# Performance work log

Hardware: AMD Instinct MI355X
Metric: run time of the kernel (lower is better)

## Reference

```python
import jax, jax.numpy as jnp
import numpy as np

ALPHA = 0.2  # tf.nn.leaky_relu default

def leaky(x):
    return jnp.where(x >= 0, x, ALPHA * x)

def segment_softmax(score, seg, num_segments):
    m = jax.ops.segment_max(score, seg, num_segments=num_segments)
    e = jnp.exp(score - m[seg])
    denom = jax.ops.segment_sum(e, seg, num_segments=num_segments)
    return e / denom[seg]

def setup_inputs() -> dict:
    key = jax.random.key(0)
    ks = jax.random.split(key, 8)
    E, NE, NR, D, U = 500000, 100000, 1000, 128, 128
    return {
        "h_index": jax.random.randint(ks[0], (E,), 0, NE),
        "r_index": jax.random.randint(ks[1], (E,), 0, NR),
        "t_index": jax.random.randint(ks[2], (E,), 0, NE),
        "entity_embeddings": jax.random.normal(ks[3], (NE, D), jnp.float32),
        "relation_embeddings": jax.random.normal(ks[4], (NR, D), jnp.float32),
        "W": jax.random.normal(ks[5], (3 * D, U), jnp.float32) * 0.05,
        "a": jax.random.normal(ks[6], (U, 1), jnp.float32) * 0.1,
        "a_b": jnp.zeros((1,), jnp.float32),
        "bias": jnp.zeros((U,), jnp.float32),
    }

def reference(h_index, r_index, t_index, entity_embeddings, relation_embeddings, W, a, a_b, bias):
    num_entities = entity_embeddings.shape[0]
    h = entity_embeddings[h_index]          # [E, D]
    r = relation_embeddings[r_index]        # [E, D]
    t = entity_embeddings[t_index]          # [E, D]
    feats = jnp.concatenate([h, r, t], axis=-1) @ W  # [E, U]
    # att_kernel Dense(1, activation=leaky_relu), then wrapped again in att_activation
    score = leaky(leaky(feats @ a + a_b))[:, 0]      # [E]
    alpha = segment_softmax(score, h_index, num_entities)
    msg = feats * alpha[:, None]                     # gcn_mapper: edge features * weight
    reduced = jax.ops.segment_sum(msg, h_index, num_segments=num_entities)  # [NE, U]
    out = reduced + bias                             # identity_updater returns reduced_msg
    return jax.nn.relu(out)
```

## Files before the change

### kernel.cpp

```cpp
#include <hip/hip_runtime.h>
#include <hip/hip_bf16.h>

#define ALPHA2 0.04f

typedef __attribute__((ext_vector_type(8))) short short8;
typedef __attribute__((ext_vector_type(4))) float floatx4;
typedef __attribute__((ext_vector_type(8))) unsigned short ushort8;

__device__ __forceinline__ unsigned short f2bf(float f) {
    unsigned u = __float_as_uint(f);
    unsigned r = (u + 0x7fffu + ((u >> 16) & 1u)) >> 16;
    return (unsigned short)r;
}
__device__ __forceinline__ float bf2f(unsigned short h) {
    return __uint_as_float((unsigned)h << 16);
}

__global__ void k_prep(const float* __restrict__ W, unsigned short* __restrict__ Wt,
                       int* __restrict__ count, int NE) {
    int idx = blockIdx.x * blockDim.x + threadIdx.x;
    if (idx < 384 * 128) {
        int k = idx >> 7, n = idx & 127;
        Wt[n * 384 + k] = f2bf(W[idx]);
    }
    if (idx < NE) count[idx] = 0;
}

#define LDA 136

__device__ __forceinline__ void gemm_phase(
        const unsigned short* Ash, unsigned short* Wsh,
        int rowbase, int nrows, int wave, int lane, int tid,
        const float* __restrict__ avec,
        unsigned short* __restrict__ OutB, float* __restrict__ svec) {
    int m16 = lane & 15, quad = lane >> 4;
    int rs = wave * 32;

    floatx4 acc[2][8];
    #pragma unroll
    for (int i = 0; i < 2; ++i)
        #pragma unroll
        for (int j = 0; j < 8; ++j) acc[i][j] = (floatx4){0.f, 0.f, 0.f, 0.f};

    #pragma unroll
    for (int kc = 0; kc < 4; ++kc) {
        short8 af[2], bf[8];
        #pragma unroll
        for (int i = 0; i < 2; ++i)
            af[i] = *(const short8*)(Ash + (rs + i * 16 + m16) * LDA + kc * 32 + quad * 8);
        #pragma unroll
        for (int j = 0; j < 8; ++j)
            bf[j] = *(const short8*)(Wsh + (j * 16 + m16) * LDA + kc * 32 + quad * 8);
        #pragma unroll
        for (int i = 0; i < 2; ++i)
            #pragma unroll
            for (int j = 0; j < 8; ++j)
                acc[i][j] = __builtin_amdgcn_mfma_f32_16x16x32_bf16(af[i], bf[j], acc[i][j], 0, 0, 0);
    }

    float av[8];
    #pragma unroll
    for (int j = 0; j < 8; ++j) av[j] = avec[j * 16 + m16];
    #pragma unroll
    for (int i = 0; i < 2; ++i) {
        #pragma unroll
        for (int reg = 0; reg < 4; ++reg) {
            int row = rowbase + rs + i * 16 + quad * 4 + reg;
            float part = 0.f;
            #pragma unroll
            for (int j = 0; j < 8; ++j) part = fmaf(acc[i][j][reg], av[j], part);
            #pragma unroll
            for (int off = 1; off < 16; off <<= 1) part += __shfl_xor(part, off);
            if (row < nrows && m16 == 0) svec[row] = part;
        }
    }

    __syncthreads();
    #pragma unroll
    for (int i = 0; i < 2; ++i)
        #pragma unroll
        for (int reg = 0; reg < 4; ++reg) {
            int lrow = rs + i * 16 + quad * 4 + reg;
            #pragma unroll
            for (int j = 0; j < 8; ++j)
                Wsh[lrow * LDA + j * 16 + m16] = f2bf(acc[i][j][reg]);
        }
    __syncthreads();
    #pragma unroll
    for (int it = 0; it < 8; ++it) {
        int id = it * 256 + tid;
        int chunk = id & 15, row = id >> 4;
        int grow = rowbase + row;
        if (grow < nrows) {
            ushort8 v = *(const ushort8*)(Wsh + row * LDA + chunk * 8);
            *(ushort8*)(OutB + (size_t)grow * 128 + chunk * 8) = v;
        }
    }
}

template <bool TWO>
__global__ __launch_bounds__(256) void k_gemm(
        const float* __restrict__ In,
        const unsigned short* __restrict__ Wt,
        int woffA, unsigned short* __restrict__ OutA, float* __restrict__ svecA,
        int woffB, unsigned short* __restrict__ OutB, float* __restrict__ svecB,
        int nrows, const float* __restrict__ avec) {
    __shared__ unsigned short Ash[128 * LDA];
    __shared__ unsigned short Wsh[128 * LDA];
    int tid = threadIdx.x;
    int rowbase = blockIdx.x * 128;
    int wave = tid >> 6, lane = tid & 63;

    #pragma unroll
    for (int it = 0; it < 16; ++it) {
        int id = it * 256 + tid;
        int chunk = id & 31, row = id >> 5;
        int grow = rowbase + row;
        if (grow > nrows - 1) grow = nrows - 1;
        float4 v = *(const float4*)(In + (size_t)grow * 128 + chunk * 4);
        ushort4 u = make_ushort4(f2bf(v.x), f2bf(v.y), f2bf(v.z), f2bf(v.w));
        *(ushort4*)(Ash + row * LDA + chunk * 4) = u;
    }
    #pragma unroll
    for (int it = 0; it < 8; ++it) {
        int id = it * 256 + tid;
        int chunk = id & 15, n = id >> 4;
        uint4 v = *(const uint4*)(Wt + (size_t)n * 384 + woffA + chunk * 8);
        *(uint4*)(Wsh + n * LDA + chunk * 8) = v;
    }
    __syncthreads();
    gemm_phase(Ash, Wsh, rowbase, nrows, wave, lane, tid, avec, OutA, svecA);

    if (TWO) {
        __syncthreads();
        #pragma unroll
        for (int it = 0; it < 8; ++it) {
            int id = it * 256 + tid;
            int chunk = id & 15, n = id >> 4;
            uint4 v = *(const uint4*)(Wt + (size_t)n * 384 + woffB + chunk * 8);
            *(uint4*)(Wsh + n * LDA + chunk * 8) = v;
        }
        __syncthreads();
        gemm_phase(Ash, Wsh, rowbase, nrows, wave, lane, tid, avec, OutB, svecB);
    }
}

__global__ void k_count(const int* __restrict__ h, int* __restrict__ count,
                        int* __restrict__ rank, int E) {
    int e = blockIdx.x * blockDim.x + threadIdx.x;
    if (e < E) rank[e] = atomicAdd(count + h[e], 1);
}

__device__ __forceinline__ int block_incl_scan256(int s, int* sh, int t) {
    sh[t] = s; __syncthreads();
    #pragma unroll
    for (int off = 1; off < 256; off <<= 1) {
        int x = 0;
        if (t >= off) x = sh[t - off];
        __syncthreads();
        sh[t] += x;
        __syncthreads();
    }
    return sh[t];
}

__global__ __launch_bounds__(256) void k_scan_a(const int* __restrict__ count, int NE,
                                                int* __restrict__ bsum) {
    __shared__ int sh[256];
    int b = blockIdx.x, t = threadIdx.x;
    int base = b * 1024 + t * 4, s = 0;
    #pragma unroll
    for (int j = 0; j < 4; ++j) { int i = base + j; if (i < NE) s += count[i]; }
    sh[t] = s; __syncthreads();
    for (int off = 128; off > 0; off >>= 1) {
        if (t < off) sh[t] += sh[t + off];
        __syncthreads();
    }
    if (t == 0) bsum[b] = sh[0];
}

__global__ __launch_bounds__(256) void k_scan_b(int* __restrict__ bsum, int NB) {
    __shared__ int sh[256];
    int t = threadIdx.x;
    int v[4]; int s = 0;
    #pragma unroll
    for (int j = 0; j < 4; ++j) { int i = t * 4 + j; v[j] = (i < NB) ? bsum[i] : 0; s += v[j]; }
    int incl = block_incl_scan256(s, sh, t);
    int excl = incl - s;
    #pragma unroll
    for (int j = 0; j < 4; ++j) {
        int i = t * 4 + j;
        if (i < NB) { int tmp = v[j]; bsum[i] = excl; excl += tmp; }
    }
}

__global__ __launch_bounds__(256) void k_scan_c(const int* __restrict__ count, int NE,
                                                const int* __restrict__ bsum,
                                                int* __restrict__ rowstart, int E) {
    __shared__ int sh[256];
    int b = blockIdx.x, t = threadIdx.x;
    int base = b * 1024 + t * 4;
    int v[4]; int s = 0;
    #pragma unroll
    for (int j = 0; j < 4; ++j) { int i = base + j; v[j] = (i < NE) ? count[i] : 0; s += v[j]; }
    int incl = block_incl_scan256(s, sh, t);
    int excl = bsum[b] + incl - s;
    #pragma unroll
    for (int j = 0; j < 4; ++j) {
        int i = base + j;
        if (i < NE) { rowstart[i] = excl; excl += v[j]; }
    }
    if (b == 0 && t == 0) rowstart[NE] = E;
}

__global__ void k_score_scatter(const int* __restrict__ h, const int* __restrict__ r,
                                const int* __restrict__ t, const float* __restrict__ s1,
                                const float* __restrict__ s2, const float* __restrict__ s3,
                                const float* __restrict__ a_b,
                                const int* __restrict__ rowstart, const int* __restrict__ rank,
                                uint2* __restrict__ rt_s, int E) {
    int e = blockIdx.x * blockDim.x + threadIdx.x;
    if (e >= E) return;
    int hi = h[e], ri = r[e], ti = t[e];
    float x = s1[hi] + s2[ri] + s3[ti] + a_b[0];
    float sc = (x >= 0.f) ? x : ALPHA2 * x;
    float ev = __expf(sc);
    rt_s[rowstart[hi] + rank[e]] = make_uint2(((unsigned)ri << 17) | (unsigned)ti,
                                              __float_as_uint(ev));
}

__global__ __launch_bounds__(256) void k_aggregate(const int* __restrict__ rowstart,
                                                   const uint2* __restrict__ rt_s,
                                                   const unsigned short* __restrict__ Pb,
                                                   const unsigned short* __restrict__ Qb,
                                                   const unsigned short* __restrict__ Rb,
                                                   const float* __restrict__ bias,
                                                   float* __restrict__ out, int NE) {
    int gid = blockIdx.x * blockDim.x + threadIdx.x;
    int n = gid >> 4;
    int sl = gid & 15;
    if (n >= NE) return;
    int start = rowstart[n], end = rowstart[n + 1];
    int c0 = sl * 8;
    float acc[8] = {};
    float evsum = 0.f;
    int i = start;
    for (; i + 2 <= end; i += 2) {
        uint2 m0 = rt_s[i], m1 = rt_s[i + 1];
        float ev0 = __uint_as_float(m0.y), ev1 = __uint_as_float(m1.y);
        unsigned t0 = m0.x & 0x1FFFFu, r0 = m0.x >> 17;
        unsigned t1 = m1.x & 0x1FFFFu, r1 = m1.x >> 17;
        ushort8 q0 = *(const ushort8*)(Qb + (size_t)t0 * 128 + c0);
        ushort8 rr0 = *(const ushort8*)(Rb + (size_t)r0 * 128 + c0);
        ushort8 q1 = *(const ushort8*)(Qb + (size_t)t1 * 128 + c0);
        ushort8 rr1 = *(const ushort8*)(Rb + (size_t)r1 * 128 + c0);
        evsum += ev0 + ev1;
        #pragma unroll
        for (int j = 0; j < 8; ++j)
            acc[j] = fmaf(ev0, bf2f(q0[j]) + bf2f(rr0[j]), acc[j]);
        #pragma unroll
        for (int j = 0; j < 8; ++j)
            acc[j] = fmaf(ev1, bf2f(q1[j]) + bf2f(rr1[j]), acc[j]);
    }
    if (i < end) {
        uint2 m0 = rt_s[i];
        float ev0 = __uint_as_float(m0.y);
        unsigned t0 = m0.x & 0x1FFFFu, r0 = m0.x >> 17;
        ushort8 q0 = *(const ushort8*)(Qb + (size_t)t0 * 128 + c0);
        ushort8 rr0 = *(const ushort8*)(Rb + (size_t)r0 * 128 + c0);
        evsum += ev0;
        #pragma unroll
        for (int j = 0; j < 8; ++j)
            acc[j] = fmaf(ev0, bf2f(q0[j]) + bf2f(rr0[j]), acc[j]);
    }
    float4 b0 = *(const float4*)(bias + c0);
    float4 b1 = *(const float4*)(bias + c0 + 4);
    float bi[8] = {b0.x, b0.y, b0.z, b0.w, b1.x, b1.y, b1.z, b1.w};
    float o[8];
    if (end > start) {
        float inv = 1.f / evsum;
        ushort8 pb = *(const ushort8*)(Pb + (size_t)n * 128 + c0);
        #pragma unroll
        for (int j = 0; j < 8; ++j) o[j] = bf2f(pb[j]) + acc[j] * inv + bi[j];
    } else {
        #pragma unroll
        for (int j = 0; j < 8; ++j) o[j] = bi[j];
    }
    #pragma unroll
    for (int j = 0; j < 8; ++j) o[j] = fmaxf(o[j], 0.f);
    float* op = out + (size_t)n * 128 + c0;
    *(float4*)(op)     = make_float4(o[0], o[1], o[2], o[3]);
    *(float4*)(op + 4) = make_float4(o[4], o[5], o[6], o[7]);
}

static inline size_t align_up(size_t x, size_t a) { return (x + a - 1) / a * a; }

extern "C" void kernel_launch(void* const* d_in, const int* in_sizes, int n_in,
                              void* d_out, int out_size, void* d_ws, size_t ws_size,
                              hipStream_t stream) {
    const int* h_index = (const int*)d_in[0];
    const int* r_index = (const int*)d_in[1];
    const int* t_index = (const int*)d_in[2];
    const float* ent = (const float*)d_in[3];
    const float* rel = (const float*)d_in[4];
    const float* W = (const float*)d_in[5];
    const float* a = (const float*)d_in[6];
    const float* a_b = (const float*)d_in[7];
    const float* bias = (const float*)d_in[8];
    float* out = (float*)d_out;

    int E = in_sizes[0];
    int NE = in_sizes[3] / 128;
    int NR = in_sizes[4] / 128;

    char* p = (char*)d_ws;
    auto alloc = [&](size_t bytes) { char* q = p; p += align_up(bytes, 256); return (void*)q; };
    unsigned short* Pb = (unsigned short*)alloc((size_t)NE * 128 * 2);
    unsigned short* Qb = (unsigned short*)alloc((size_t)NE * 128 * 2);
    unsigned short* Rb = (unsigned short*)alloc((size_t)NR * 128 * 2);
    unsigned short* Wt = (unsigned short*)alloc((size_t)128 * 384 * 2);
    float* s1 = (float*)alloc((size_t)NE * 4);
    float* s3 = (float*)alloc((size_t)NE * 4);
    float* s2 = (float*)alloc((size_t)NR * 4);
    int* count = (int*)alloc((size_t)NE * 4);
    int* rowstart = (int*)alloc((size_t)(NE + 1) * 4);
    int* rank = (int*)alloc((size_t)E * 4);
    int NB = (NE + 1023) / 1024;
    int* bsum = (int*)alloc((size_t)NB * 4);
    uint2* rt_s = (uint2*)alloc((size_t)E * 8);
    (void)ws_size; (void)n_in; (void)out_size;

    int nprep = (NE > 384 * 128) ? NE : 384 * 128;
    k_prep<<<(nprep + 255) / 256, 256, 0, stream>>>(W, Wt, count, NE);
    k_count<<<(E + 255) / 256, 256, 0, stream>>>(h_index, count, rank, E);
    k_gemm<true><<<(NE + 127) / 128, 256, 0, stream>>>(ent, Wt, 0, Pb, s1, 256, Qb, s3, NE, a);
    k_gemm<false><<<(NR + 127) / 128, 256, 0, stream>>>(rel, Wt, 128, Rb, s2, 0, nullptr, nullptr, NR, a);
    k_scan_a<<<NB, 256, 0, stream>>>(count, NE, bsum);
    k_scan_b<<<1, 256, 0, stream>>>(bsum, NB);
    k_scan_c<<<NB, 256, 0, stream>>>(count, NE, bsum, rowstart, E);
    k_score_scatter<<<(E + 255) / 256, 256, 0, stream>>>(h_index, r_index, t_index,
                                                         s1, s2, s3, a_b, rowstart,
                                                         rank, rt_s, E);
    k_aggregate<<<(NE * 16 + 255) / 256, 256, 0, stream>>>(rowstart, rt_s, Pb, Qb, Rb,
                                                           bias, out, NE);
}
```

Measured before the change: 216.5 us.

## Merge GEMM launches, preload W fragments, store outputs in permuted column order

W is pre-arranged into MFMA B-fragment order once, so each wave loads its B operands straight from global or cache instead of staging W through shared memory. The entity and relation GEMMs become a single launch with 4-block occupancy bounds. Outputs are written directly from registers in a column-permuted layout, skipping the shared-memory transpose round-trip. The aggregate kernel reads bias and writes output with the matching permutation. In exchange, every block re-reads W fragments from global memory, and the final output stores become strided scalar writes.

```diff
diff --git a/kernel.cpp b/kernel.cpp
--- a/kernel.cpp
+++ b/kernel.cpp
@@ -2,6 +2,7 @@
 #include <hip/hip_bf16.h>
 
 #define ALPHA2 0.04f
+#define LDA 136
 
 typedef __attribute__((ext_vector_type(8))) short short8;
 typedef __attribute__((ext_vector_type(4))) float floatx4;
@@ -16,100 +17,33 @@
     return __uint_as_float((unsigned)h << 16);
 }
 
-__global__ void k_prep(const float* __restrict__ W, unsigned short* __restrict__ Wt,
+
+__global__ void k_prep(const float* __restrict__ W, unsigned short* __restrict__ Bfr,
                        int* __restrict__ count, int NE) {
     int idx = blockIdx.x * blockDim.x + threadIdx.x;
-    if (idx < 384 * 128) {
-        int k = idx >> 7, n = idx & 127;
-        Wt[n * 384 + k] = f2bf(W[idx]);
+    if (idx < 3 * 128 * 128) {
+        int kk = idx & 7, n = (idx >> 3) & 127, g = idx >> 10;
+        int slice = g >> 4, kc = (g >> 2) & 3, quad = g & 3;
+        int k = kc * 32 + quad * 8 + kk;
+        Bfr[idx] = f2bf(W[(size_t)(slice * 128 + k) * 128 + n]);
     }
     if (idx < NE) count[idx] = 0;
 }
 
-#define LDA 136
-
-__device__ __forceinline__ void gemm_phase(
-        const unsigned short* Ash, unsigned short* Wsh,
-        int rowbase, int nrows, int wave, int lane, int tid,
-        const float* __restrict__ avec,
-        unsigned short* __restrict__ OutB, float* __restrict__ svec) {
-    int m16 = lane & 15, quad = lane >> 4;
-    int rs = wave * 32;
-
-    floatx4 acc[2][8];
-    #pragma unroll
-    for (int i = 0; i < 2; ++i)
-        #pragma unroll
-        for (int j = 0; j < 8; ++j) acc[i][j] = (floatx4){0.f, 0.f, 0.f, 0.f};
-
-    #pragma unroll
-    for (int kc = 0; kc < 4; ++kc) {
-        short8 af[2], bf[8];
-        #pragma unroll
-        for (int i = 0; i < 2; ++i)
-            af[i] = *(const short8*)(Ash + (rs + i * 16 + m16) * LDA + kc * 32 + quad * 8);
-        #pragma unroll
-        for (int j = 0; j < 8; ++j)
-            bf[j] = *(const short8*)(Wsh + (j * 16 + m16) * LDA + kc * 32 + quad * 8);
-        #pragma unroll
-        for (int i = 0; i < 2; ++i)
-            #pragma unroll
-            for (int j = 0; j < 8; ++j)
-                acc[i][j] = __builtin_amdgcn_mfma_f32_16x16x32_bf16(af[i], bf[j], acc[i][j], 0, 0, 0);
-    }
-
-    float av[8];
-    #pragma unroll
-    for (int j = 0; j < 8; ++j) av[j] = avec[j * 16 + m16];
-    #pragma unroll
-    for (int i = 0; i < 2; ++i) {
-        #pragma unroll
-        for (int reg = 0; reg < 4; ++reg) {
-            int row = rowbase + rs + i * 16 + quad * 4 + reg;
-            float part = 0.f;
-            #pragma unroll
-            for (int j = 0; j < 8; ++j) part = fmaf(acc[i][j][reg], av[j], part);
-            #pragma unroll
-            for (int off = 1; off < 16; off <<= 1) part += __shfl_xor(part, off);
-            if (row < nrows && m16 == 0) svec[row] = part;
-        }
-    }
-
-    __syncthreads();
-    #pragma unroll
-    for (int i = 0; i < 2; ++i)
-        #pragma unroll
-        for (int reg = 0; reg < 4; ++reg) {
-            int lrow = rs + i * 16 + quad * 4 + reg;
-            #pragma unroll
-            for (int j = 0; j < 8; ++j)
-                Wsh[lrow * LDA + j * 16 + m16] = f2bf(acc[i][j][reg]);
-        }
-    __syncthreads();
-    #pragma unroll
-    for (int it = 0; it < 8; ++it) {
-        int id = it * 256 + tid;
-        int chunk = id & 15, row = id >> 4;
-        int grow = rowbase + row;
-        if (grow < nrows) {
-            ushort8 v = *(const ushort8*)(Wsh + row * LDA + chunk * 8);
-            *(ushort8*)(OutB + (size_t)grow * 128 + chunk * 8) = v;
-        }
-    }
-}
-
-template <bool TWO>
-__global__ __launch_bounds__(256) void k_gemm(
-        const float* __restrict__ In,
-        const unsigned short* __restrict__ Wt,
-        int woffA, unsigned short* __restrict__ OutA, float* __restrict__ svecA,
-        int woffB, unsigned short* __restrict__ OutB, float* __restrict__ svecB,
-        int nrows, const float* __restrict__ avec) {
+__global__ __launch_bounds__(256, 4) void k_gemm_all(
+        const float* __restrict__ ent, const float* __restrict__ rel,
+        const unsigned short* __restrict__ Bfr,
+        unsigned short* __restrict__ Pb, unsigned short* __restrict__ Qb,
+        unsigned short* __restrict__ Rb,
+        float* __restrict__ s1, float* __restrict__ s3, float* __restrict__ s2,
+        const float* __restrict__ avec, int NE, int NR, int NBent) {
     __shared__ unsigned short Ash[128 * LDA];
-    __shared__ unsigned short Wsh[128 * LDA];
     int tid = threadIdx.x;
-    int rowbase = blockIdx.x * 128;
-    int wave = tid >> 6, lane = tid & 63;
+    int b = blockIdx.x;
+    bool isEnt = b < NBent;
+    const float* In = isEnt ? ent : rel;
+    int nrows = isEnt ? NE : NR;
+    int rowbase = (isEnt ? b : b - NBent) * 128;
 
     #pragma unroll
     for (int it = 0; it < 16; ++it) {
@@ -121,27 +55,65 @@
         ushort4 u = make_ushort4(f2bf(v.x), f2bf(v.y), f2bf(v.z), f2bf(v.w));
         *(ushort4*)(Ash + row * LDA + chunk * 4) = u;
     }
-    #pragma unroll
-    for (int it = 0; it < 8; ++it) {
-        int id = it * 256 + tid;
-        int chunk = id & 15, n = id >> 4;
-        uint4 v = *(const uint4*)(Wt + (size_t)n * 384 + woffA + chunk * 8);
-        *(uint4*)(Wsh + n * LDA + chunk * 8) = v;
-    }
     __syncthreads();
-    gemm_phase(Ash, Wsh, rowbase, nrows, wave, lane, tid, avec, OutA, svecA);
-
-    if (TWO) {
-        __syncthreads();
-        #pragma unroll
-        for (int it = 0; it < 8; ++it) {
-            int id = it * 256 + tid;
-            int chunk = id & 15, n = id >> 4;
-            uint4 v = *(const uint4*)(Wt + (size_t)n * 384 + woffB + chunk * 8);
-            *(uint4*)(Wsh + n * LDA + chunk * 8) = v;
+
+    int wave = tid >> 6, lane = tid & 63;
+    int m16 = lane & 15, quad = lane >> 4;
+    int rs = wave * 32;
+
+    float av[8];
+    #pragma unroll
+    for (int j = 0; j < 8; ++j) av[j] = avec[j * 16 + m16];
+
+    int nphase = isEnt ? 2 : 1;
+    for (int ph = 0; ph < nphase; ++ph) {
+        int slice; unsigned short* Out; float* svec;
+        if (isEnt) { slice = ph ? 2 : 0; Out = ph ? Qb : Pb; svec = ph ? s3 : s1; }
+        else       { slice = 1; Out = Rb; svec = s2; }
+
+        floatx4 acc[2][8];
+        #pragma unroll
+        for (int i = 0; i < 2; ++i)
+            #pragma unroll
+            for (int j = 0; j < 8; ++j) acc[i][j] = (floatx4){0.f, 0.f, 0.f, 0.f};
+
+        #pragma unroll
+        for (int kc = 0; kc < 4; ++kc) {
+            const unsigned short* bb = Bfr + (size_t)((slice * 4 + kc) * 4 + quad) * 1024 + m16 * 8;
+            short8 bf[8], af[2];
+            #pragma unroll
+            for (int j = 0; j < 8; ++j) bf[j] = *(const short8*)(bb + j * 128);
+            #pragma unroll
+            for (int i = 0; i < 2; ++i)
+                af[i] = *(const short8*)(Ash + (rs + i * 16 + m16) * LDA + kc * 32 + quad * 8);
+            #pragma unroll
+            for (int i = 0; i < 2; ++i)
+                #pragma unroll
+                for (int j = 0; j < 8; ++j)
+                    acc[i][j] = __builtin_amdgcn_mfma_f32_16x16x32_bf16(af[i], bf[j], acc[i][j], 0, 0, 0);
         }
-        __syncthreads();
-        gemm_phase(Ash, Wsh, rowbase, nrows, wave, lane, tid, avec, OutB, svecB);
+
+        #pragma unroll
+        for (int i = 0; i < 2; ++i) {
+            #pragma unroll
+            for (int reg = 0; reg < 4; ++reg) {
+                int row = rowbase + rs + i * 16 + quad * 4 + reg;
+                float part = 0.f;
+                ushort8 v;
+                #pragma unroll
+                for (int j = 0; j < 8; ++j) {
+                    float x = acc[i][j][reg];
+                    part = fmaf(x, av[j], part);
+                    v[j] = f2bf(x);
+                }
+                #pragma unroll
+                for (int off = 1; off < 16; off <<= 1) part += __shfl_xor(part, off);
+                if (row < nrows) {
+                    *(ushort8*)(Out + (size_t)row * 128 + m16 * 8) = v;
+                    if (m16 == 0) svec[row] = part;
+                }
+            }
+        }
     }
 }
 
@@ -273,9 +245,9 @@
         for (int j = 0; j < 8; ++j)
             acc[j] = fmaf(ev0, bf2f(q0[j]) + bf2f(rr0[j]), acc[j]);
     }
-    float4 b0 = *(const float4*)(bias + c0);
-    float4 b1 = *(const float4*)(bias + c0 + 4);
-    float bi[8] = {b0.x, b0.y, b0.z, b0.w, b1.x, b1.y, b1.z, b1.w};
+    float bi[8];
+    #pragma unroll
+    for (int j = 0; j < 8; ++j) bi[j] = bias[j * 16 + sl];
     float o[8];
     if (end > start) {
         float inv = 1.f / evsum;
@@ -287,10 +259,8 @@
         for (int j = 0; j < 8; ++j) o[j] = bi[j];
     }
     #pragma unroll
-    for (int j = 0; j < 8; ++j) o[j] = fmaxf(o[j], 0.f);
-    float* op = out + (size_t)n * 128 + c0;
-    *(float4*)(op)     = make_float4(o[0], o[1], o[2], o[3]);
-    *(float4*)(op + 4) = make_float4(o[4], o[5], o[6], o[7]);
+    for (int j = 0; j < 8; ++j)
+        out[(size_t)n * 128 + j * 16 + sl] = fmaxf(o[j], 0.f);
 }
 
 static inline size_t align_up(size_t x, size_t a) { return (x + a - 1) / a * a; }
@@ -318,7 +288,7 @@
     unsigned short* Pb = (unsigned short*)alloc((size_t)NE * 128 * 2);
     unsigned short* Qb = (unsigned short*)alloc((size_t)NE * 128 * 2);
     unsigned short* Rb = (unsigned short*)alloc((size_t)NR * 128 * 2);
-    unsigned short* Wt = (unsigned short*)alloc((size_t)128 * 384 * 2);
+    unsigned short* Bfr = (unsigned short*)alloc((size_t)3 * 128 * 128 * 2);
     float* s1 = (float*)alloc((size_t)NE * 4);
     float* s3 = (float*)alloc((size_t)NE * 4);
     float* s2 = (float*)alloc((size_t)NR * 4);
@@ -330,11 +300,12 @@
     uint2* rt_s = (uint2*)alloc((size_t)E * 8);
     (void)ws_size; (void)n_in; (void)out_size;
 
-    int nprep = (NE > 384 * 128) ? NE : 384 * 128;
-    k_prep<<<(nprep + 255) / 256, 256, 0, stream>>>(W, Wt, count, NE);
+    int nprep = (NE > 3 * 128 * 128) ? NE : 3 * 128 * 128;
+    k_prep<<<(nprep + 255) / 256, 256, 0, stream>>>(W, Bfr, count, NE);
     k_count<<<(E + 255) / 256, 256, 0, stream>>>(h_index, count, rank, E);
-    k_gemm<true><<<(NE + 127) / 128, 256, 0, stream>>>(ent, Wt, 0, Pb, s1, 256, Qb, s3, NE, a);
-    k_gemm<false><<<(NR + 127) / 128, 256, 0, stream>>>(rel, Wt, 128, Rb, s2, 0, nullptr, nullptr, NR, a);
+    int NBent = (NE + 127) / 128, NBrel = (NR + 127) / 128;
+    k_gemm_all<<<NBent + NBrel, 256, 0, stream>>>(ent, rel, Bfr, Pb, Qb, Rb,
+                                                  s1, s3, s2, a, NE, NR, NBent);
     k_scan_a<<<NB, 256, 0, stream>>>(count, NE, bsum);
     k_scan_b<<<1, 256, 0, stream>>>(bsum, NB);
     k_scan_c<<<NB, 256, 0, stream>>>(count, NE, bsum, rowstart, E);
```

After: 221.0 us. 1.02x slower.
